# Performance work log

Hardware: AMD Instinct MI355X
Metric: run time of the kernel (lower is better)

The kernel has to match this reference:

```python
import jax, jax.numpy as jnp
import numpy as np

ENC_DIM = 128
DEC_DIM = 128
NUM_HEADS = 4
HEAD_DIM = DEC_DIM // NUM_HEADS


def _layernorm(x, g, b, eps=1e-5):
    mu = jnp.mean(x, axis=-1, keepdims=True)
    var = jnp.mean((x - mu) ** 2, axis=-1, keepdims=True)
    return (x - mu) * jax.lax.rsqrt(var + eps) * g + b


def setup_inputs() -> dict:
    key = jax.random.key(0)
    ks = jax.random.split(key, 12)
    B, H, W, D = 2, 16, 16, 16
    s = 0.02
    return {
        "encoder_feat": jax.random.normal(ks[0], (B, ENC_DIM, H, W, D), jnp.float32),
        "decoder_feat": jax.random.normal(ks[1], (B, DEC_DIM, H, W, D), jnp.float32),
        # torch Linear weights stored as [out, in]
        "Wq": jax.random.normal(ks[2], (DEC_DIM, DEC_DIM), jnp.float32) * s,
        "bq": jnp.zeros((DEC_DIM,), jnp.float32),
        "Wk": jax.random.normal(ks[3], (DEC_DIM, ENC_DIM), jnp.float32) * s,
        "bk": jnp.zeros((DEC_DIM,), jnp.float32),
        "Wv": jax.random.normal(ks[4], (DEC_DIM, ENC_DIM), jnp.float32) * s,
        "bv": jnp.zeros((DEC_DIM,), jnp.float32),
        "Wo": jax.random.normal(ks[5], (DEC_DIM, DEC_DIM), jnp.float32) * s,
        "bo": jnp.zeros((DEC_DIM,), jnp.float32),
        "g_enc": jnp.ones((ENC_DIM,), jnp.float32),
        "b_enc": jnp.zeros((ENC_DIM,), jnp.float32),
        "g_dec": jnp.ones((DEC_DIM,), jnp.float32),
        "b_dec": jnp.zeros((DEC_DIM,), jnp.float32),
        "g_out": jnp.ones((DEC_DIM,), jnp.float32),
        "b_out": jnp.zeros((DEC_DIM,), jnp.float32),
        "W1": jax.random.normal(ks[6], (DEC_DIM * 4, DEC_DIM), jnp.float32) * s,
        "b1": jnp.zeros((DEC_DIM * 4,), jnp.float32),
        "W2": jax.random.normal(ks[7], (DEC_DIM, DEC_DIM * 4), jnp.float32) * s,
        "b2": jnp.zeros((DEC_DIM,), jnp.float32),
    }


def reference(encoder_feat, decoder_feat, Wq, bq, Wk, bk, Wv, bv, Wo, bo,
              g_enc, b_enc, g_dec, b_dec, g_out, b_out, W1, b1, W2, b2):
    B, C_dec, H, W_, D = decoder_feat.shape
    N = H * W_ * D
    scale = HEAD_DIM ** -0.5
    # [B, C, H, W, D] -> [B, N, C]
    enc_seq = encoder_feat.reshape(B, -1, N).transpose(0, 2, 1)
    dec_seq = decoder_feat.reshape(B, C_dec, N).transpose(0, 2, 1)
    enc_seq = _layernorm(enc_seq, g_enc, b_enc)
    dec_seq = _layernorm(dec_seq, g_dec, b_dec)
    # projections (torch Linear: x @ W.T + b), split heads -> [B, h, N, d]
    Q = (dec_seq @ Wq.T + bq).reshape(B, N, NUM_HEADS, HEAD_DIM).transpose(0, 2, 1, 3)
    K = (enc_seq @ Wk.T + bk).reshape(B, N, NUM_HEADS, HEAD_DIM).transpose(0, 2, 1, 3)
    V = (enc_seq @ Wv.T + bv).reshape(B, N, NUM_HEADS, HEAD_DIM).transpose(0, 2, 1, 3)
    attn = jnp.einsum('bhqd,bhkd->bhqk', Q, K) * scale  # [B, h, N, N]
    attn = jax.nn.softmax(attn, axis=-1)
    out = jnp.einsum('bhqk,bhkd->bhqd', attn, V)
    out = out.transpose(0, 2, 1, 3).reshape(B, N, C_dec)
    out = out @ Wo.T + bo
    out = dec_seq + out
    h = _layernorm(out, g_out, b_out)
    ffn = jax.nn.gelu(h @ W1.T + b1, approximate=False) @ W2.T + b2
    out = out + ffn
    return out.transpose(0, 2, 1).reshape(B, C_dec, H, W_, D)
```

## Files before the change

kernel.cpp:

```cpp
#include <hip/hip_runtime.h>
#include <hip/hip_bf16.h>
#include <math.h>

#define B_ 2
#define N_ 4096
#define BN_ 8192
#define NH_ 4
#define SPLIT_ 8

using bf16x8   = __attribute__((ext_vector_type(8))) __bf16;
using f32x4    = __attribute__((ext_vector_type(4))) float;
using ushortx8 = __attribute__((ext_vector_type(8))) unsigned short;

#if __has_builtin(__builtin_amdgcn_exp2f)
#define FAST_EXP2(x) __builtin_amdgcn_exp2f(x)
#else
#define FAST_EXP2(x) __expf((x) * 0.6931471805599453f)
#endif

static __device__ __forceinline__ unsigned short f2bf(float f) {
    union { __hip_bfloat16 h; unsigned short u; } c;
    c.h = __float2bfloat16(f);
    return c.u;
}
static __device__ __forceinline__ float bf2f(unsigned short u) {
    union { __hip_bfloat16 h; unsigned short u; } c;
    c.u = u;
    return __bfloat162float(c.h);
}
static __device__ __forceinline__ unsigned int pk2bf(float lo, float hi) {
    return __builtin_amdgcn_perm(__float_as_uint(hi) + 0x8000u,
                                 __float_as_uint(lo) + 0x8000u, 0x07060302u);
}

__global__ __launch_bounds__(256)
void convert_weights_kernel(const float* __restrict__ Wq, const float* __restrict__ Wk,
                            const float* __restrict__ Wv, const float* __restrict__ Wo,
                            const float* __restrict__ W1, const float* __restrict__ W2,
                            unsigned short* __restrict__ wq, unsigned short* __restrict__ wk,
                            unsigned short* __restrict__ wv, unsigned short* __restrict__ wo,
                            unsigned short* __restrict__ w1, unsigned short* __restrict__ w2) {
    const int id = blockIdx.x * 256 + threadIdx.x;
    if      (id <  16384) wq[id]          = f2bf(Wq[id]);
    else if (id <  32768) wk[id - 16384]  = f2bf(Wk[id - 16384]);
    else if (id <  49152) wv[id - 32768]  = f2bf(Wv[id - 32768]);
    else if (id <  65536) wo[id - 49152]  = f2bf(Wo[id - 49152]);
    else if (id < 131072) w1[id - 65536]  = f2bf(W1[id - 65536]);
    else                  w2[id - 131072] = f2bf(W2[id - 131072]);
}

__global__ __launch_bounds__(256)
void ln_transpose_kernel(const float* __restrict__ enc, const float* __restrict__ dec,
                         const float* __restrict__ g_enc, const float* __restrict__ b_enc,
                         const float* __restrict__ g_dec, const float* __restrict__ b_dec,
                         unsigned short* __restrict__ enc_out,
                         unsigned short* __restrict__ dec_out) {
    __shared__ float tile[128][33];
    __shared__ float mu_s[32], inv_s[32];
    const int z  = blockIdx.z;
    const float* in     = z ? dec   : enc;
    const float* gamma  = z ? g_dec : g_enc;
    const float* beta   = z ? b_dec : b_enc;
    unsigned short* outb = z ? dec_out : enc_out;
    const int b  = blockIdx.y;
    const int n0 = blockIdx.x * 32;
    const int t  = threadIdx.x;
    const float* inb = in + (size_t)b * 128 * N_;

    {
        const int col = t & 31;
        const int r0  = t >> 5;
        for (int j = 0; j < 16; ++j) {
            const int r = r0 + 8 * j;
            tile[r][col] = inb[(size_t)r * N_ + n0 + col];
        }
    }
    __syncthreads();
    {
        const int tok = t >> 3;
        const int ln  = t & 7;
        float s = 0.f, ss = 0.f;
        for (int c = ln; c < 128; c += 8) {
            const float x = tile[c][tok];
            s += x; ss += x * x;
        }
        for (int m = 1; m < 8; m <<= 1) {
            s  += __shfl_xor(s, m);
            ss += __shfl_xor(ss, m);
        }
        if (ln == 0) {
            const float mu  = s * (1.f / 128.f);
            const float var = ss * (1.f / 128.f) - mu * mu;
            mu_s[tok]  = mu;
            inv_s[tok] = rsqrtf(var + 1e-5f);
        }
    }
    __syncthreads();
    const size_t obase = ((size_t)b * N_ + n0) * 128;
    for (int j = 0; j < 16; ++j) {
        const int f  = t + 256 * j;
        const int tk = f >> 7;
        const int c  = f & 127;
        const float x = tile[c][tk];
        outb[obase + f] = f2bf((x - mu_s[tk]) * inv_s[tk] * gamma[c] + beta[c]);
    }
}

__global__ __launch_bounds__(128)
void qkv_gemm_kernel(const unsigned short* __restrict__ decb,
                     const unsigned short* __restrict__ encb,
                     const unsigned short* __restrict__ wq,
                     const unsigned short* __restrict__ wk,
                     const unsigned short* __restrict__ wv,
                     const float* __restrict__ bq, const float* __restrict__ bk,
                     const float* __restrict__ bv,
                     unsigned short* __restrict__ Qh, unsigned short* __restrict__ Kh,
                     unsigned short* __restrict__ Vt) {
    const int z = blockIdx.y;
    const int t = threadIdx.x;
    const int wvx = t >> 6, lane = t & 63;
    const int l15 = lane & 15, quad = lane >> 4;
    const int m0 = blockIdx.x * 32 + wvx * 16;
    const unsigned short* X    = (z == 0) ? decb : encb;
    const unsigned short* Wb   = (z == 0) ? wq : (z == 1) ? wk : wv;
    const float*          bias = (z == 0) ? bq : (z == 1) ? bk : bv;

    bf16x8 af[4];
    #pragma unroll
    for (int kk = 0; kk < 4; ++kk)
        af[kk] = *(const bf16x8*)(X + (size_t)(m0 + l15) * 128 + kk * 32 + quad * 8);

    f32x4 acc[8];
    #pragma unroll
    for (int nb = 0; nb < 8; ++nb) {
        f32x4 a = {0.f, 0.f, 0.f, 0.f};
        #pragma unroll
        for (int kk = 0; kk < 4; ++kk) {
            const bf16x8 wf = *(const bf16x8*)(Wb + (size_t)(nb * 16 + l15) * 128 + kk * 32 + quad * 8);
            a = __builtin_amdgcn_mfma_f32_16x16x32_bf16(af[kk], wf, a, 0, 0, 0);
        }
        acc[nb] = a;
    }

    const float qsc = 0.17677669529663687f * 1.4426950408889634f;
    const int b   = m0 >> 12;
    const int nb0 = (m0 & 4095) + quad * 4;
    #pragma unroll
    for (int nb = 0; nb < 8; ++nb) {
        const int col = nb * 16 + l15;
        const int h = col >> 5, d = col & 31;
        const float bz = bias[col];
        if (z == 2) {
            ushort4 pk;
            pk.x = f2bf(acc[nb][0] + bz);
            pk.y = f2bf(acc[nb][1] + bz);
            pk.z = f2bf(acc[nb][2] + bz);
            pk.w = f2bf(acc[nb][3] + bz);
            *(ushort4*)(Vt + ((size_t)(b * NH_ + h) * 32 + d) * N_ + nb0) = pk;
        } else {
            unsigned short* dst = (z == 0) ? Qh : Kh;
            const float sc = (z == 0) ? qsc : 1.f;
            #pragma unroll
            for (int r = 0; r < 4; ++r) {
                const int n = nb0 + r;
                dst[((size_t)(b * NH_ + h) * N_ + n) * 32 + d] = f2bf((acc[nb][r] + bz) * sc);
            }
        }
    }
}

__global__ __launch_bounds__(256)
void attn_kernel5(const unsigned short* __restrict__ Qh,
                  const unsigned short* __restrict__ Kh,
                  const unsigned short* __restrict__ Vt,
                  unsigned short* __restrict__ Op,
                  unsigned short* __restrict__ lp) {
    __shared__ alignas(16) unsigned short sP[4][64][72];

    const int gid   = blockIdx.x;
    const int combo = gid & 63;
    const int qblk  = gid >> 6;
    const int bh    = combo & 7;
    const int s     = combo >> 3;
    const int t  = threadIdx.x;
    const int wvx = t >> 6, lane = t & 63;
    const int l15 = lane & 15, quad = lane >> 4;
    const int qw = qblk * 256 + wvx * 64;
    const size_t hbse = (size_t)bh * N_ * 32;

    bf16x8 qf[4];
    #pragma unroll
    for (int f = 0; f < 4; ++f)
        qf[f] = *(const bf16x8*)(Qh + hbse + (size_t)(qw + f * 16 + l15) * 32 + quad * 8);

    const unsigned short* Kp = Kh + hbse;
    const unsigned short* Vp = Vt + (size_t)bh * 32 * N_;

    f32x4 o0[4], o1[4];
    float l[4];
    #pragma unroll
    for (int f = 0; f < 4; ++f) {
        o0[f] = f32x4{0.f, 0.f, 0.f, 0.f};
        o1[f] = f32x4{0.f, 0.f, 0.f, 0.f};
        l[f] = 0.f;
    }
    const f32x4 zero = {0.f, 0.f, 0.f, 0.f};

    const int kbeg = s * (N_ / SPLIT_);
    const int kend = kbeg + (N_ / SPLIT_);

    bf16x8 kf[4];
    #pragma unroll
    for (int c = 0; c < 4; ++c)
        kf[c] = *(const bf16x8*)(Kp + (size_t)(kbeg + c * 16 + l15) * 32 + quad * 8);

    for (int k0 = kbeg; k0 < kend; k0 += 64) {
        bf16x8 va[2], vb[2];
        #pragma unroll
        for (int s2 = 0; s2 < 2; ++s2) {
            va[s2] = *(const bf16x8*)(Vp + (size_t)l15 * N_        + k0 + s2 * 32 + quad * 8);
            vb[s2] = *(const bf16x8*)(Vp + (size_t)(16 + l15) * N_ + k0 + s2 * 32 + quad * 8);
        }
        const int kn = (k0 + 64 < kend) ? (k0 + 64) : kbeg;
        bf16x8 kfn[4];
        #pragma unroll
        for (int c = 0; c < 4; ++c)
            kfn[c] = *(const bf16x8*)(Kp + (size_t)(kn + c * 16 + l15) * 32 + quad * 8);

        #pragma unroll
        for (int f = 0; f < 4; ++f) {
            #pragma unroll
            for (int c = 0; c < 4; ++c) {
                const f32x4 sv = __builtin_amdgcn_mfma_f32_16x16x32_bf16(kf[c], qf[f], zero, 0, 0, 0);
                const float p0 = FAST_EXP2(sv[0]);
                const float p1 = FAST_EXP2(sv[1]);
                const float p2 = FAST_EXP2(sv[2]);
                const float p3 = FAST_EXP2(sv[3]);
                l[f] += (p0 + p1) + (p2 + p3);
                uint2 pk;
                pk.x = pk2bf(p0, p1);
                pk.y = pk2bf(p2, p3);
                *(uint2*)&sP[wvx][f * 16 + l15][c * 16 + quad * 4] = pk;
            }
        }
        #pragma unroll
        for (int f = 0; f < 4; ++f) {
            #pragma unroll
            for (int s2 = 0; s2 < 2; ++s2) {
                const bf16x8 pf = *(const bf16x8*)&sP[wvx][f * 16 + l15][s2 * 32 + quad * 8];
                o0[f] = __builtin_amdgcn_mfma_f32_16x16x32_bf16(va[s2], pf, o0[f], 0, 0, 0);
                o1[f] = __builtin_amdgcn_mfma_f32_16x16x32_bf16(vb[s2], pf, o1[f], 0, 0, 0);
            }
        }
        #pragma unroll
        for (int c = 0; c < 4; ++c) kf[c] = kfn[c];
    }

    #pragma unroll
    for (int f = 0; f < 4; ++f) {
        float lf = l[f];
        lf += __shfl_xor(lf, 16);
        lf += __shfl_xor(lf, 32);
        const int tok = qw + f * 16 + l15;
        const size_t ob = ((size_t)(s * 8 + bh) * N_ + tok) * 32;
        uint2 w0, w1v;
        w0.x  = pk2bf(o0[f][0], o0[f][1]); w0.y  = pk2bf(o0[f][2], o0[f][3]);
        w1v.x = pk2bf(o1[f][0], o1[f][1]); w1v.y = pk2bf(o1[f][2], o1[f][3]);
        *(uint2*)&Op[ob + quad * 4]      = w0;
        *(uint2*)&Op[ob + 16 + quad * 4] = w1v;
        if (quad == 0)
            lp[(size_t)(s * 8 + bh) * N_ + tok] = f2bf(lf);
    }
}

__global__ __launch_bounds__(256)
void combine_kernel(const unsigned short* __restrict__ Op,
                    const unsigned short* __restrict__ lp,
                    unsigned short* __restrict__ ctx) {
    const int gid = blockIdx.x * 256 + threadIdx.x;
    const int token = gid >> 4;
    const int c8 = gid & 15;
    const int b = token >> 12, n = token & 4095;
    const int h = c8 >> 2;
    const int d0 = (c8 & 3) * 8;
    const int bh = b * NH_ + h;

    f32x4 sa = {0.f, 0.f, 0.f, 0.f}, sb = {0.f, 0.f, 0.f, 0.f};
    float lt = 0.f;
    #pragma unroll
    for (int s = 0; s < SPLIT_; ++s) {
        const size_t base = ((size_t)(s * 8 + bh) * N_ + n) * 32 + d0;
        const ushortx8 u = *(const ushortx8*)&Op[base];
        sa[0] += bf2f(u[0]); sa[1] += bf2f(u[1]);
        sa[2] += bf2f(u[2]); sa[3] += bf2f(u[3]);
        sb[0] += bf2f(u[4]); sb[1] += bf2f(u[5]);
        sb[2] += bf2f(u[6]); sb[3] += bf2f(u[7]);
        lt += bf2f(lp[(size_t)(s * 8 + bh) * N_ + n]);
    }
    const float inv = 1.f / lt;
    uint4 pk;
    pk.x = pk2bf(sa[0] * inv, sa[1] * inv);
    pk.y = pk2bf(sa[2] * inv, sa[3] * inv);
    pk.z = pk2bf(sb[0] * inv, sb[1] * inv);
    pk.w = pk2bf(sb[2] * inv, sb[3] * inv);
    *(uint4*)(ctx + (size_t)token * 128 + c8 * 8) = pk;
}

__global__ __launch_bounds__(256)
void wo_gemm_kernel(const unsigned short* __restrict__ ctx,
                    const unsigned short* __restrict__ wo,
                    const float* __restrict__ bo,
                    const unsigned short* __restrict__ decb,
                    const float* __restrict__ g, const float* __restrict__ be,
                    unsigned short* __restrict__ out1,
                    unsigned short* __restrict__ hb) {
    __shared__ alignas(16) float sred[2][64][32];
    const int t = threadIdx.x;
    const int wvx = t >> 6, lane = t & 63;
    const int pair = wvx >> 1, kh = wvx & 1;
    const int l15 = lane & 15, quad = lane >> 4;
    const int m0 = blockIdx.x * 32 + pair * 16;

    bf16x8 af[2];
    #pragma unroll
    for (int kk = 0; kk < 2; ++kk)
        af[kk] = *(const bf16x8*)(ctx + (size_t)(m0 + l15) * 128 + (kh * 2 + kk) * 32 + quad * 8);

    float v[8][4];
    #pragma unroll
    for (int nb = 0; nb < 8; ++nb) {
        f32x4 a = {0.f, 0.f, 0.f, 0.f};
        #pragma unroll
        for (int kk = 0; kk < 2; ++kk) {
            const bf16x8 wf = *(const bf16x8*)(wo + (size_t)(nb * 16 + l15) * 128 + (kh * 2 + kk) * 32 + quad * 8);
            a = __builtin_amdgcn_mfma_f32_16x16x32_bf16(af[kk], wf, a, 0, 0, 0);
        }
        #pragma unroll
        for (int r = 0; r < 4; ++r) v[nb][r] = a[r];
    }

    if (kh == 1) {
        #pragma unroll
        for (int nb = 0; nb < 8; ++nb)
            *(f32x4*)&sred[pair][lane][nb * 4] = *(f32x4*)&v[nb][0];
    }
    __syncthreads();
    if (kh == 0) {
        #pragma unroll
        for (int nb = 0; nb < 8; ++nb) {
            const f32x4 p = *(const f32x4*)&sred[pair][lane][nb * 4];
            const int col = nb * 16 + l15;
            const float bz = bo[col];
            #pragma unroll
            for (int r = 0; r < 4; ++r) {
                const int tok = m0 + quad * 4 + r;
                v[nb][r] += p[r] + bz + bf2f(decb[(size_t)tok * 128 + col]);
            }
        }
        float mu[4], inv[4];
        #pragma unroll
        for (int r = 0; r < 4; ++r) {
            float s = 0.f, ss = 0.f;
            #pragma unroll
            for (int nb = 0; nb < 8; ++nb) { s += v[nb][r]; ss += v[nb][r] * v[nb][r]; }
            for (int m = 1; m < 16; m <<= 1) {
                s  += __shfl_xor(s, m);
                ss += __shfl_xor(ss, m);
            }
            mu[r] = s * (1.f / 128.f);
            inv[r] = rsqrtf(ss * (1.f / 128.f) - mu[r] * mu[r] + 1e-5f);
        }
        #pragma unroll
        for (int nb = 0; nb < 8; ++nb) {
            const int col = nb * 16 + l15;
            const float gg = g[col], bb2 = be[col];
            #pragma unroll
            for (int r = 0; r < 4; ++r) {
                const int tok = m0 + quad * 4 + r;
                out1[(size_t)tok * 128 + col] = f2bf(v[nb][r]);
                hb[(size_t)tok * 128 + col]   = f2bf((v[nb][r] - mu[r]) * inv[r] * gg + bb2);
            }
        }
    }
}

__global__ __launch_bounds__(128)
void ffn1_kernel(const unsigned short* __restrict__ hb,
                 const unsigned short* __restrict__ w1,
                 const float* __restrict__ b1,
                 unsigned short* __restrict__ midb) {
    const int t = threadIdx.x;
    const int wvx = t >> 6, lane = t & 63;
    const int l15 = lane & 15, quad = lane >> 4;
    const int m0 = blockIdx.x * 32 + wvx * 16;
    const int nbase = blockIdx.y * 128;

    bf16x8 af[4];
    #pragma unroll
    for (int kk = 0; kk < 4; ++kk)
        af[kk] = *(const bf16x8*)(hb + (size_t)(m0 + l15) * 128 + kk * 32 + quad * 8);

    #pragma unroll
    for (int nb = 0; nb < 8; ++nb) {
        f32x4 a = {0.f, 0.f, 0.f, 0.f};
        const int col = nbase + nb * 16 + l15;
        #pragma unroll
        for (int kk = 0; kk < 4; ++kk) {
            const bf16x8 wf = *(const bf16x8*)(w1 + (size_t)col * 128 + kk * 32 + quad * 8);
            a = __builtin_amdgcn_mfma_f32_16x16x32_bf16(af[kk], wf, a, 0, 0, 0);
        }
        const float bz = b1[col];
        #pragma unroll
        for (int r = 0; r < 4; ++r) {
            const int tok = m0 + quad * 4 + r;
            float x = a[r] + bz;
            x = 0.5f * x * (1.f + erff(x * 0.70710678118f));
            midb[(size_t)tok * 512 + col] = f2bf(x);
        }
    }
}

__global__ __launch_bounds__(256)
void ffn2_kernel(const unsigned short* __restrict__ midb,
                 const unsigned short* __restrict__ w2,
                 const float* __restrict__ b2,
                 const unsigned short* __restrict__ out1,
                 float* __restrict__ out) {
    __shared__ alignas(16) float sred[2][64][32];
    const int t = threadIdx.x;
    const int wvx = t >> 6, lane = t & 63;
    const int pair = wvx >> 1, kh = wvx & 1;
    const int l15 = lane & 15, quad = lane >> 4;
    const int m0 = blockIdx.x * 32 + pair * 16;

    bf16x8 af[8];
    #pragma unroll
    for (int kk = 0; kk < 8; ++kk)
        af[kk] = *(const bf16x8*)(midb + (size_t)(m0 + l15) * 512 + (kh * 8 + kk) * 32 + quad * 8);

    float v[8][4];
    #pragma unroll
    for (int nb = 0; nb < 8; ++nb) {
        f32x4 a = {0.f, 0.f, 0.f, 0.f};
        const int col = nb * 16 + l15;
        #pragma unroll
        for (int kk = 0; kk < 8; ++kk) {
            const bf16x8 wf = *(const bf16x8*)(w2 + (size_t)col * 512 + (kh * 8 + kk) * 32 + quad * 8);
            a = __builtin_amdgcn_mfma_f32_16x16x32_bf16(af[kk], wf, a, 0, 0, 0);
        }
        #pragma unroll
        for (int r = 0; r < 4; ++r) v[nb][r] = a[r];
    }

    if (kh == 1) {
        #pragma unroll
        for (int nb = 0; nb < 8; ++nb)
            *(f32x4*)&sred[pair][lane][nb * 4] = *(f32x4*)&v[nb][0];
    }
    __syncthreads();
    if (kh == 0) {
        const int b = m0 >> 12;
        const int nb0 = (m0 & 4095) + quad * 4;
        #pragma unroll
        for (int nb = 0; nb < 8; ++nb) {
            const f32x4 p = *(const f32x4*)&sred[pair][lane][nb * 4];
            const int col = nb * 16 + l15;
            const float bz = b2[col];
            f32x4 res;
            #pragma unroll
            for (int r = 0; r < 4; ++r) {
                const int tok = m0 + quad * 4 + r;
                res[r] = v[nb][r] + p[r] + bz + bf2f(out1[(size_t)tok * 128 + col]);
            }
            *(f32x4*)&out[((size_t)(b * 128 + col)) * N_ + nb0] = res;
        }
    }
}

extern "C" void kernel_launch(void* const* d_in, const int* in_sizes, int n_in,
                              void* d_out, int out_size, void* d_ws, size_t ws_size,
                              hipStream_t stream) {
    const float* enc   = (const float*)d_in[0];
    const float* dec   = (const float*)d_in[1];
    const float* Wq    = (const float*)d_in[2];
    const float* bq    = (const float*)d_in[3];
    const float* Wk    = (const float*)d_in[4];
    const float* bk    = (const float*)d_in[5];
    const float* Wv    = (const float*)d_in[6];
    const float* bv    = (const float*)d_in[7];
    const float* Wo    = (const float*)d_in[8];
    const float* bo    = (const float*)d_in[9];
    const float* g_enc = (const float*)d_in[10];
    const float* b_enc = (const float*)d_in[11];
    const float* g_dec = (const float*)d_in[12];
    const float* b_dec = (const float*)d_in[13];
    const float* g_out = (const float*)d_in[14];
    const float* b_out = (const float*)d_in[15];
    const float* W1    = (const float*)d_in[16];
    const float* b1    = (const float*)d_in[17];
    const float* W2    = (const float*)d_in[18];
    const float* b2    = (const float*)d_in[19];
    float* out = (float*)d_out;
    char*  W   = (char*)d_ws;

    unsigned short* wqb = (unsigned short*)(W);
    unsigned short* wkb = wqb + 16384;
    unsigned short* wvb = wkb + 16384;
    unsigned short* wob = wvb + 16384;
    unsigned short* w1b = wob + 16384;
    unsigned short* w2b = w1b + 65536;
    unsigned short* enc_lnb = (unsigned short*)(W + (512ull  << 10));
    unsigned short* dec_lnb = (unsigned short*)(W + (2560ull << 10));
    unsigned short* Qh      = (unsigned short*)(W + (4608ull << 10));
    unsigned short* Kh      = (unsigned short*)(W + (6656ull << 10));
    unsigned short* Vt      = (unsigned short*)(W + (8704ull << 10));
    unsigned short* Op      = (unsigned short*)(W + (10752ull << 10));
    unsigned short* lpb     = (unsigned short*)(W + (27136ull << 10));
    unsigned short* ctx  = enc_lnb;
    unsigned short* out1 = Qh;
    unsigned short* hbuf = Kh;
    unsigned short* midb = Op;

    convert_weights_kernel<<<768, 256, 0, stream>>>(Wq, Wk, Wv, Wo, W1, W2,
                                                    wqb, wkb, wvb, wob, w1b, w2b);

    ln_transpose_kernel<<<dim3(N_ / 32, B_, 2), 256, 0, stream>>>(
        enc, dec, g_enc, b_enc, g_dec, b_dec, enc_lnb, dec_lnb);

    qkv_gemm_kernel<<<dim3(BN_ / 32, 3), 128, 0, stream>>>(
        dec_lnb, enc_lnb, wqb, wkb, wvb, bq, bk, bv, Qh, Kh, Vt);

    attn_kernel5<<<1024, 256, 0, stream>>>(Qh, Kh, Vt, Op, lpb);

    combine_kernel<<<512, 256, 0, stream>>>(Op, lpb, ctx);

    wo_gemm_kernel<<<BN_ / 32, 256, 0, stream>>>(ctx, wob, bo, dec_lnb, g_out, b_out,
                                                 out1, hbuf);

    ffn1_kernel<<<dim3(BN_ / 32, 4), 128, 0, stream>>>(hbuf, w1b, b1, midb);

    ffn2_kernel<<<BN_ / 32, 256, 0, stream>>>(midb, w2b, b2, out1, out);
}
```

Measured before the change: 187.7 us.

## Fuse split-K combine, Wo, LayerNorm and FFN into one tail kernel; shrink attention tiles

Merges the split-K combine, output projection with residual and LayerNorm, FFN1 with GELU, and FFN2 with residual into one kernel. Intermediates stay in LDS and registers, which removes four launches and the global round trips for ctx, out1, hbuf and the 512-wide mid activation. Separately, the attention kernel now gives each wave 32 queries instead of 64, doubling the grid to 2048 blocks for more parallelism at the cost of reloading K/V more often. The fused tail runs 256 blocks of 256 threads and does serial FFN work per block, so it may have low occupancy.

```diff
diff --git a/kernel.cpp b/kernel.cpp
--- a/kernel.cpp
+++ b/kernel.cpp
@@ -170,12 +170,12 @@
 }
 
 __global__ __launch_bounds__(256)
-void attn_kernel5(const unsigned short* __restrict__ Qh,
+void attn_kernel6(const unsigned short* __restrict__ Qh,
                   const unsigned short* __restrict__ Kh,
                   const unsigned short* __restrict__ Vt,
                   unsigned short* __restrict__ Op,
                   unsigned short* __restrict__ lp) {
-    __shared__ alignas(16) unsigned short sP[4][64][72];
+    __shared__ alignas(16) unsigned short sP[4][32][72];
 
     const int gid   = blockIdx.x;
     const int combo = gid & 63;
@@ -185,21 +185,21 @@
     const int t  = threadIdx.x;
     const int wvx = t >> 6, lane = t & 63;
     const int l15 = lane & 15, quad = lane >> 4;
-    const int qw = qblk * 256 + wvx * 64;
+    const int qw = qblk * 128 + wvx * 32;
     const size_t hbse = (size_t)bh * N_ * 32;
 
-    bf16x8 qf[4];
-    #pragma unroll
-    for (int f = 0; f < 4; ++f)
+    bf16x8 qf[2];
+    #pragma unroll
+    for (int f = 0; f < 2; ++f)
         qf[f] = *(const bf16x8*)(Qh + hbse + (size_t)(qw + f * 16 + l15) * 32 + quad * 8);
 
     const unsigned short* Kp = Kh + hbse;
     const unsigned short* Vp = Vt + (size_t)bh * 32 * N_;
 
-    f32x4 o0[4], o1[4];
-    float l[4];
-    #pragma unroll
-    for (int f = 0; f < 4; ++f) {
+    f32x4 o0[2], o1[2];
+    float l[2];
+    #pragma unroll
+    for (int f = 0; f < 2; ++f) {
         o0[f] = f32x4{0.f, 0.f, 0.f, 0.f};
         o1[f] = f32x4{0.f, 0.f, 0.f, 0.f};
         l[f] = 0.f;
@@ -228,7 +228,7 @@
             kfn[c] = *(const bf16x8*)(Kp + (size_t)(kn + c * 16 + l15) * 32 + quad * 8);
 
         #pragma unroll
-        for (int f = 0; f < 4; ++f) {
+        for (int f = 0; f < 2; ++f) {
             #pragma unroll
             for (int c = 0; c < 4; ++c) {
                 const f32x4 sv = __builtin_amdgcn_mfma_f32_16x16x32_bf16(kf[c], qf[f], zero, 0, 0, 0);
@@ -244,7 +244,7 @@
             }
         }
         #pragma unroll
-        for (int f = 0; f < 4; ++f) {
+        for (int f = 0; f < 2; ++f) {
             #pragma unroll
             for (int s2 = 0; s2 < 2; ++s2) {
                 const bf16x8 pf = *(const bf16x8*)&sP[wvx][f * 16 + l15][s2 * 32 + quad * 8];
@@ -257,7 +257,7 @@
     }
 
     #pragma unroll
-    for (int f = 0; f < 4; ++f) {
+    for (int f = 0; f < 2; ++f) {
         float lf = l[f];
         lf += __shfl_xor(lf, 16);
         lf += __shfl_xor(lf, 32);
@@ -274,77 +274,73 @@
 }
 
 __global__ __launch_bounds__(256)
-void combine_kernel(const unsigned short* __restrict__ Op,
-                    const unsigned short* __restrict__ lp,
-                    unsigned short* __restrict__ ctx) {
-    const int gid = blockIdx.x * 256 + threadIdx.x;
-    const int token = gid >> 4;
-    const int c8 = gid & 15;
-    const int b = token >> 12, n = token & 4095;
-    const int h = c8 >> 2;
-    const int d0 = (c8 & 3) * 8;
-    const int bh = b * NH_ + h;
-
-    f32x4 sa = {0.f, 0.f, 0.f, 0.f}, sb = {0.f, 0.f, 0.f, 0.f};
-    float lt = 0.f;
-    #pragma unroll
-    for (int s = 0; s < SPLIT_; ++s) {
-        const size_t base = ((size_t)(s * 8 + bh) * N_ + n) * 32 + d0;
-        const ushortx8 u = *(const ushortx8*)&Op[base];
-        sa[0] += bf2f(u[0]); sa[1] += bf2f(u[1]);
-        sa[2] += bf2f(u[2]); sa[3] += bf2f(u[3]);
-        sb[0] += bf2f(u[4]); sb[1] += bf2f(u[5]);
-        sb[2] += bf2f(u[6]); sb[3] += bf2f(u[7]);
-        lt += bf2f(lp[(size_t)(s * 8 + bh) * N_ + n]);
-    }
-    const float inv = 1.f / lt;
-    uint4 pk;
-    pk.x = pk2bf(sa[0] * inv, sa[1] * inv);
-    pk.y = pk2bf(sa[2] * inv, sa[3] * inv);
-    pk.z = pk2bf(sb[0] * inv, sb[1] * inv);
-    pk.w = pk2bf(sb[2] * inv, sb[3] * inv);
-    *(uint4*)(ctx + (size_t)token * 128 + c8 * 8) = pk;
-}
-
-__global__ __launch_bounds__(256)
-void wo_gemm_kernel(const unsigned short* __restrict__ ctx,
-                    const unsigned short* __restrict__ wo,
-                    const float* __restrict__ bo,
-                    const unsigned short* __restrict__ decb,
-                    const float* __restrict__ g, const float* __restrict__ be,
-                    unsigned short* __restrict__ out1,
-                    unsigned short* __restrict__ hb) {
+void fused_tail_kernel(const unsigned short* __restrict__ Op,
+                       const unsigned short* __restrict__ lp,
+                       const unsigned short* __restrict__ wo,
+                       const float* __restrict__ bo,
+                       const unsigned short* __restrict__ decb,
+                       const float* __restrict__ g, const float* __restrict__ be,
+                       const unsigned short* __restrict__ w1,
+                       const float* __restrict__ b1,
+                       const unsigned short* __restrict__ w2,
+                       const float* __restrict__ b2,
+                       float* __restrict__ out) {
     __shared__ alignas(16) float sred[2][64][32];
+    __shared__ alignas(16) unsigned short hb_lds[32][136];
+    __shared__ alignas(16) unsigned short smid[2][16][536];
     const int t = threadIdx.x;
     const int wvx = t >> 6, lane = t & 63;
     const int pair = wvx >> 1, kh = wvx & 1;
     const int l15 = lane & 15, quad = lane >> 4;
     const int m0 = blockIdx.x * 32 + pair * 16;
 
+    const int tokA = m0 + l15;
+    const int bA = tokA >> 12, nA = tokA & 4095;
     bf16x8 af[2];
     #pragma unroll
-    for (int kk = 0; kk < 2; ++kk)
-        af[kk] = *(const bf16x8*)(ctx + (size_t)(m0 + l15) * 128 + (kh * 2 + kk) * 32 + quad * 8);
+    for (int kkl = 0; kkl < 2; ++kkl) {
+        const int bhh = bA * NH_ + kh * 2 + kkl;
+        f32x4 sa = {0.f, 0.f, 0.f, 0.f}, sb = {0.f, 0.f, 0.f, 0.f};
+        float lt = 0.f;
+        #pragma unroll
+        for (int s = 0; s < SPLIT_; ++s) {
+            const size_t base = ((size_t)(s * 8 + bhh) * N_ + nA) * 32 + quad * 8;
+            const ushortx8 u = *(const ushortx8*)&Op[base];
+            sa[0] += bf2f(u[0]); sa[1] += bf2f(u[1]);
+            sa[2] += bf2f(u[2]); sa[3] += bf2f(u[3]);
+            sb[0] += bf2f(u[4]); sb[1] += bf2f(u[5]);
+            sb[2] += bf2f(u[6]); sb[3] += bf2f(u[7]);
+            lt += bf2f(lp[(size_t)(s * 8 + bhh) * N_ + nA]);
+        }
+        const float inv = 1.f / lt;
+        union { uint4 u; bf16x8 v; } cvt;
+        cvt.u.x = pk2bf(sa[0] * inv, sa[1] * inv);
+        cvt.u.y = pk2bf(sa[2] * inv, sa[3] * inv);
+        cvt.u.z = pk2bf(sb[0] * inv, sb[1] * inv);
+        cvt.u.w = pk2bf(sb[2] * inv, sb[3] * inv);
+        af[kkl] = cvt.v;
+    }
 
     float v[8][4];
     #pragma unroll
     for (int nb = 0; nb < 8; ++nb) {
         f32x4 a = {0.f, 0.f, 0.f, 0.f};
         #pragma unroll
-        for (int kk = 0; kk < 2; ++kk) {
-            const bf16x8 wf = *(const bf16x8*)(wo + (size_t)(nb * 16 + l15) * 128 + (kh * 2 + kk) * 32 + quad * 8);
-            a = __builtin_amdgcn_mfma_f32_16x16x32_bf16(af[kk], wf, a, 0, 0, 0);
+        for (int kkl = 0; kkl < 2; ++kkl) {
+            const bf16x8 wf = *(const bf16x8*)(wo + (size_t)(nb * 16 + l15) * 128
+                                               + (kh * 2 + kkl) * 32 + quad * 8);
+            a = __builtin_amdgcn_mfma_f32_16x16x32_bf16(af[kkl], wf, a, 0, 0, 0);
         }
         #pragma unroll
         for (int r = 0; r < 4; ++r) v[nb][r] = a[r];
     }
-
     if (kh == 1) {
         #pragma unroll
         for (int nb = 0; nb < 8; ++nb)
             *(f32x4*)&sred[pair][lane][nb * 4] = *(f32x4*)&v[nb][0];
     }
     __syncthreads();
+
     if (kh == 0) {
         #pragma unroll
         for (int nb = 0; nb < 8; ++nb) {
@@ -375,87 +371,53 @@
             const int col = nb * 16 + l15;
             const float gg = g[col], bb2 = be[col];
             #pragma unroll
-            for (int r = 0; r < 4; ++r) {
-                const int tok = m0 + quad * 4 + r;
-                out1[(size_t)tok * 128 + col] = f2bf(v[nb][r]);
-                hb[(size_t)tok * 128 + col]   = f2bf((v[nb][r] - mu[r]) * inv[r] * gg + bb2);
-            }
-        }
-    }
-}
-
-__global__ __launch_bounds__(128)
-void ffn1_kernel(const unsigned short* __restrict__ hb,
-                 const unsigned short* __restrict__ w1,
-                 const float* __restrict__ b1,
-                 unsigned short* __restrict__ midb) {
-    const int t = threadIdx.x;
-    const int wvx = t >> 6, lane = t & 63;
-    const int l15 = lane & 15, quad = lane >> 4;
-    const int m0 = blockIdx.x * 32 + wvx * 16;
-    const int nbase = blockIdx.y * 128;
-
-    bf16x8 af[4];
+            for (int r = 0; r < 4; ++r)
+                hb_lds[pair * 16 + quad * 4 + r][col] =
+                    f2bf((v[nb][r] - mu[r]) * inv[r] * gg + bb2);
+        }
+    }
+    __syncthreads();
+
+    bf16x8 hf[4];
     #pragma unroll
     for (int kk = 0; kk < 4; ++kk)
-        af[kk] = *(const bf16x8*)(hb + (size_t)(m0 + l15) * 128 + kk * 32 + quad * 8);
-
-    #pragma unroll
-    for (int nb = 0; nb < 8; ++nb) {
+        hf[kk] = *(const bf16x8*)&hb_lds[pair * 16 + l15][kk * 32 + quad * 8];
+    #pragma unroll
+    for (int nb = 0; nb < 16; ++nb) {
+        const int col = kh * 256 + nb * 16 + l15;
         f32x4 a = {0.f, 0.f, 0.f, 0.f};
-        const int col = nbase + nb * 16 + l15;
         #pragma unroll
         for (int kk = 0; kk < 4; ++kk) {
             const bf16x8 wf = *(const bf16x8*)(w1 + (size_t)col * 128 + kk * 32 + quad * 8);
-            a = __builtin_amdgcn_mfma_f32_16x16x32_bf16(af[kk], wf, a, 0, 0, 0);
+            a = __builtin_amdgcn_mfma_f32_16x16x32_bf16(hf[kk], wf, a, 0, 0, 0);
         }
         const float bz = b1[col];
         #pragma unroll
         for (int r = 0; r < 4; ++r) {
-            const int tok = m0 + quad * 4 + r;
             float x = a[r] + bz;
             x = 0.5f * x * (1.f + erff(x * 0.70710678118f));
-            midb[(size_t)tok * 512 + col] = f2bf(x);
-        }
-    }
-}
-
-__global__ __launch_bounds__(256)
-void ffn2_kernel(const unsigned short* __restrict__ midb,
-                 const unsigned short* __restrict__ w2,
-                 const float* __restrict__ b2,
-                 const unsigned short* __restrict__ out1,
-                 float* __restrict__ out) {
-    __shared__ alignas(16) float sred[2][64][32];
-    const int t = threadIdx.x;
-    const int wvx = t >> 6, lane = t & 63;
-    const int pair = wvx >> 1, kh = wvx & 1;
-    const int l15 = lane & 15, quad = lane >> 4;
-    const int m0 = blockIdx.x * 32 + pair * 16;
-
-    bf16x8 af[8];
-    #pragma unroll
-    for (int kk = 0; kk < 8; ++kk)
-        af[kk] = *(const bf16x8*)(midb + (size_t)(m0 + l15) * 512 + (kh * 8 + kk) * 32 + quad * 8);
-
-    float v[8][4];
-    #pragma unroll
-    for (int nb = 0; nb < 8; ++nb) {
-        f32x4 a = {0.f, 0.f, 0.f, 0.f};
-        const int col = nb * 16 + l15;
-        #pragma unroll
-        for (int kk = 0; kk < 8; ++kk) {
-            const bf16x8 wf = *(const bf16x8*)(w2 + (size_t)col * 512 + (kh * 8 + kk) * 32 + quad * 8);
-            a = __builtin_amdgcn_mfma_f32_16x16x32_bf16(af[kk], wf, a, 0, 0, 0);
-        }
-        #pragma unroll
-        for (int r = 0; r < 4; ++r) v[nb][r] = a[r];
-    }
-
+            smid[pair][quad * 4 + r][col] = f2bf(x);
+        }
+    }
+    __syncthreads();
+
+    f32x4 acc[8];
+    #pragma unroll
+    for (int nb = 0; nb < 8; ++nb) acc[nb] = f32x4{0.f, 0.f, 0.f, 0.f};
+    #pragma unroll
+    for (int kk = 0; kk < 8; ++kk) {
+        const bf16x8 af2 = *(const bf16x8*)&smid[pair][l15][kh * 256 + kk * 32 + quad * 8];
+        #pragma unroll
+        for (int nb = 0; nb < 8; ++nb) {
+            const bf16x8 wf = *(const bf16x8*)(w2 + (size_t)(nb * 16 + l15) * 512
+                                               + kh * 256 + kk * 32 + quad * 8);
+            acc[nb] = __builtin_amdgcn_mfma_f32_16x16x32_bf16(af2, wf, acc[nb], 0, 0, 0);
+        }
+    }
     if (kh == 1) {
         #pragma unroll
         for (int nb = 0; nb < 8; ++nb)
-            *(f32x4*)&sred[pair][lane][nb * 4] = *(f32x4*)&v[nb][0];
+            *(f32x4*)&sred[pair][lane][nb * 4] = acc[nb];
     }
     __syncthreads();
     if (kh == 0) {
@@ -468,10 +430,8 @@
             const float bz = b2[col];
             f32x4 res;
             #pragma unroll
-            for (int r = 0; r < 4; ++r) {
-                const int tok = m0 + quad * 4 + r;
-                res[r] = v[nb][r] + p[r] + bz + bf2f(out1[(size_t)tok * 128 + col]);
-            }
+            for (int r = 0; r < 4; ++r)
+                res[r] = acc[nb][r] + p[r] + bz + v[nb][r];
             *(f32x4*)&out[((size_t)(b * 128 + col)) * N_ + nb0] = res;
         }
     }
@@ -516,10 +476,6 @@
     unsigned short* Vt      = (unsigned short*)(W + (8704ull << 10));
     unsigned short* Op      = (unsigned short*)(W + (10752ull << 10));
     unsigned short* lpb     = (unsigned short*)(W + (27136ull << 10));
-    unsigned short* ctx  = enc_lnb;
-    unsigned short* out1 = Qh;
-    unsigned short* hbuf = Kh;
-    unsigned short* midb = Op;
 
     convert_weights_kernel<<<768, 256, 0, stream>>>(Wq, Wk, Wv, Wo, W1, W2,
                                                     wqb, wkb, wvb, wob, w1b, w2b);
@@ -530,14 +486,8 @@
     qkv_gemm_kernel<<<dim3(BN_ / 32, 3), 128, 0, stream>>>(
         dec_lnb, enc_lnb, wqb, wkb, wvb, bq, bk, bv, Qh, Kh, Vt);
 
-    attn_kernel5<<<1024, 256, 0, stream>>>(Qh, Kh, Vt, Op, lpb);
-
-    combine_kernel<<<512, 256, 0, stream>>>(Op, lpb, ctx);
-
-    wo_gemm_kernel<<<BN_ / 32, 256, 0, stream>>>(ctx, wob, bo, dec_lnb, g_out, b_out,
-                                                 out1, hbuf);
-
-    ffn1_kernel<<<dim3(BN_ / 32, 4), 128, 0, stream>>>(hbuf, w1b, b1, midb);
-
-    ffn2_kernel<<<BN_ / 32, 256, 0, stream>>>(midb, w2b, b2, out1, out);
-}
+    attn_kernel6<<<2048, 256, 0, stream>>>(Qh, Kh, Vt, Op, lpb);
+
+    fused_tail_kernel<<<BN_ / 32, 256, 0, stream>>>(Op, lpb, wob, bo, dec_lnb,
+                                                    g_out, b_out, w1b, b1, w2b, b2, out);
+}
```

After: 192.7 us. 1.03x slower.
